# Kernel optimization log

Hardware: AMD Instinct MI355X
Metric: run time of the kernel (lower is better)

## Reference

```python
import jax, jax.numpy as jnp
import numpy as np

E, M, IN, OUT = 8, 8192, 2048, 8192


def setup_inputs() -> dict:
    key = jax.random.key(0)
    k1, k2, k3 = jax.random.split(key, 3)
    inputs = jax.random.normal(k1, (M, IN), dtype=jnp.float32)
    # truncated_normal(-3,3) scaled by init_scale/sqrt(In), matching MoELinear.init
    weight = jax.random.truncated_normal(k2, -3.0, 3.0, (E, IN, OUT), dtype=jnp.float32) * (1.0 / np.sqrt(IN))
    bias = jax.random.normal(k3, (OUT,), dtype=jnp.float32) * 0.02
    # tokens are pre-sorted by expert; balanced routing: M/E tokens per expert
    group_sizes = jnp.full((E,), M // E, dtype=jnp.int32)
    return {"inputs": inputs, "weight": weight, "group_sizes": group_sizes, "bias": bias}


def _ragged_matmul(inputs, weight, group_sizes):
    """Grouped GEMM: out[m] = inputs[m] @ weight[expert_of(m)].

    Tokens are contiguous per expert; group_sizes[e] gives the count for
    expert e. Same math as jax.lax.ragged_dot / megablox gmm.
    """
    n_experts = weight.shape[0]
    m = inputs.shape[0]
    # static-length repeat -> per-token expert id, jit-safe
    expert_ids = jnp.repeat(jnp.arange(n_experts, dtype=group_sizes.dtype),
                            group_sizes, total_repeat_length=m)  # [M]

    def body(acc, ew):
        e, w = ew  # w: [In, Out]
        mask = (expert_ids == e).astype(inputs.dtype)  # [M]
        return acc + (inputs * mask[:, None]) @ w, None

    acc0 = jnp.zeros((m, weight.shape[2]), dtype=inputs.dtype)
    out, _ = jax.lax.scan(body, acc0, (jnp.arange(n_experts, dtype=group_sizes.dtype), weight))
    return out


def reference(inputs, weight, group_sizes, bias):
    # MoELinear.__call__ (ragged_dot path): grouped matmul + bias
    return _ragged_matmul(inputs, weight, group_sizes) + bias
```

## Files before the change

### kernel.cpp

```cpp
#include <hip/hip_runtime.h>
#include <hip/hip_bf16.h>
#include <stdint.h>

#define E_ 8
#define M_ 8192
#define K_ 2048
#define N_ 8192

#define BM 256
#define BN 256
#define BK 64
#define NT (K_ / BK)
#define LDS_BYTES 131072

typedef __attribute__((ext_vector_type(8))) short bf16x8;
typedef __attribute__((ext_vector_type(4))) float f32x4;
typedef __attribute__((ext_vector_type(8))) unsigned short us8;

__device__ __forceinline__ unsigned short f2bf(float f) {
  union { float f; uint32_t u; } v; v.f = f;
  uint32_t u = v.u;
  uint32_t r = (u + 0x7FFFu + ((u >> 16) & 1u)) >> 16;
  return (unsigned short)r;
}

__device__ __forceinline__ unsigned short f2bf_hw(float f) {
  union { __hip_bfloat16 h; unsigned short u; } v;
  v.h = __float2bfloat16(f);
  return v.u;
}

__device__ __forceinline__ void gload_lds16(const void* g, void* l) {
  __builtin_amdgcn_global_load_lds(
      (const __attribute__((address_space(1))) unsigned int*)g,
      (__attribute__((address_space(3))) unsigned int*)l,
      16, 0, 0);
}

__global__ __launch_bounds__(256) void conv_a(const float* __restrict__ A,
                                              unsigned short* __restrict__ Ab,
                                              int n8) {
  int stride = gridDim.x * blockDim.x;
  for (int idx = blockIdx.x * blockDim.x + threadIdx.x; idx < n8; idx += stride) {
    const float4* p = reinterpret_cast<const float4*>(A) + (size_t)idx * 2;
    float4 x0 = p[0], x1 = p[1];
    us8 o;
    o[0] = f2bf(x0.x); o[1] = f2bf(x0.y); o[2] = f2bf(x0.z); o[3] = f2bf(x0.w);
    o[4] = f2bf(x1.x); o[5] = f2bf(x1.y); o[6] = f2bf(x1.z); o[7] = f2bf(x1.w);
    *reinterpret_cast<us8*>(Ab + (size_t)idx * 8) = o;
  }
}

__global__ __launch_bounds__(512, 2) void moe_gemm_fused(
    const unsigned short* __restrict__ Ab,
    const float* __restrict__ W,
    const int* __restrict__ gs,
    const float* __restrict__ bias,
    float* __restrict__ C) {
  extern __shared__ char smem[];

  int tile_n = blockIdx.x;
  int tile_m = blockIdx.y;

  int expert = -1, row_start = 0, rows = 0;
  {
    int acc = 0, off = 0;
    for (int e = 0; e < E_; ++e) {
      int g = gs[e];
      int t = (g + BM - 1) / BM;
      if (expert < 0 && tile_m < acc + t) {
        int lt = tile_m - acc;
        expert = e;
        row_start = off + lt * BM;
        rows = min(BM, g - lt * BM);
      }
      acc += t;
      off += g;
    }
    if (expert < 0) return;
  }

  const float* WfE = W + (size_t)expert * K_ * N_;

  int tid = threadIdx.x;
  int lane = tid & 63;
  int wave = tid >> 6;
  int wr = wave >> 2;
  int wc = wave & 3;
  int bh = wc >> 1;
  int ln15 = lane & 15;
  int n0 = tile_n * BN;

  int slot0 = (((lane >> 4) ^ ((ln15 >> 1) & 7)) << 4);
  int aBase = wr * 16384 + ln15 * 128;
  int bBase = 32768 + bh * 16384 + (wc & 1) * 8192 + ln15 * 128;

  int soff = tid * 16;
  int crow = tid >> 3;
  int lslot = (tid & 7) ^ ((crow >> 1) & 7);
  int scolA = lslot * 8;
  const unsigned short* aS[4];
  #pragma unroll
  for (int c = 0; c < 4; ++c) {
    int r = c * 64 + crow;
    int gr = r < rows ? r : 0;
    aS[c] = Ab + (size_t)(row_start + gr) * K_ + scolA;
  }
#define STG_A(DB, c, kt) \
  gload_lds16(aS[c] + (kt) * 64, smem + (DB) + (c) * 8192 + soff)

  int nB = (tid & 127) * 2;
  int kb0 = tid >> 7;
  const float* wB = WfE + (size_t)(n0 + nB);
  int sB0 = (kb0 ^ ((nB >> 1) & 7)) << 4;
  int sB1 = ((kb0 + 4) ^ ((nB >> 1) & 7)) << 4;
  int bw00 = 32768 + nB * 128 + sB0;
  int bw01 = 32768 + (nB + 1) * 128 + sB0;
  int bw10 = 32768 + nB * 128 + sB1;
  int bw11 = 32768 + (nB + 1) * 128 + sB1;

  float2 fB0[8], fB1[8];

#define LOAD_B(arr, KB, KT)                                                   \
  _Pragma("unroll") for (int j = 0; j < 8; ++j)                               \
    arr[j] = *(const float2*)(wB + (size_t)((KT) * 64 + (KB) * 8 + j) * N_);

#define CVT_WRITE(arr, WE, WO, DBN)                                           \
  do {                                                                        \
    us8 oe, oo;                                                               \
    _Pragma("unroll") for (int p = 0; p < 8; ++p) {                           \
      oe[p] = f2bf_hw(arr[p].x);                                              \
      oo[p] = f2bf_hw(arr[p].y);                                              \
    }                                                                         \
    *(us8*)(smem + (DBN) + (WE)) = oe;                                        \
    *(us8*)(smem + (DBN) + (WO)) = oo;                                        \
  } while (0)

  f32x4 acc4[8][4];
  #pragma unroll
  for (int i = 0; i < 8; ++i)
    #pragma unroll
    for (int j = 0; j < 4; ++j)
      acc4[i][j] = f32x4{0.f, 0.f, 0.f, 0.f};

#define DS_A(frag, DB, MH, KS)                                                \
  _Pragma("unroll") for (int mi = 0; mi < 4; ++mi)                            \
    frag[mi] = *(const bf16x8*)(smem + (DB) + aBase + (MH) * 8192 +           \
                                mi * 2048 + (slot0 ^ ((KS) << 6)));
#define DS_B(frag, DB, KS)                                                    \
  _Pragma("unroll") for (int nj = 0; nj < 4; ++nj)                            \
    frag[nj] = *(const bf16x8*)(smem + (DB) + bBase + nj * 2048 +             \
                                (slot0 ^ ((KS) << 6)));
#define MFMA16(MB, af, bf)                                                    \
  __builtin_amdgcn_s_setprio(1);                                              \
  _Pragma("unroll") for (int mi = 0; mi < 4; ++mi)                            \
    _Pragma("unroll") for (int nj = 0; nj < 4; ++nj)                          \
      acc4[(MB) + mi][nj] = __builtin_amdgcn_mfma_f32_16x16x32_bf16(          \
          af[mi], bf[nj], acc4[(MB) + mi][nj], 0, 0, 0);                      \
  __builtin_amdgcn_s_setprio(0);

#define TILE4(DB, DBN, KTN)                                                   \
  do {                                                                        \
    bf16x8 af[4], bf[4];                                                      \
                                                                      \
    DS_A(af, DB, 0, 0); DS_B(bf, DB, 0);                                      \
    LOAD_B(fB0, kb0, KTN);                                                    \
    __builtin_amdgcn_sched_barrier(0);                                        \
    __builtin_amdgcn_s_barrier();                                             \
    asm volatile("s_waitcnt lgkmcnt(0)" ::: "memory");                        \
    __builtin_amdgcn_sched_barrier(0);                                        \
    MFMA16(0, af, bf);                                                        \
    __builtin_amdgcn_s_barrier();                                             \
                                              \
    DS_A(af, DB, 1, 0);                                                       \
    LOAD_B(fB1, kb0 + 4, KTN);                                                \
    STG_A(DBN, 0, KTN); STG_A(DBN, 1, KTN);                                   \
    STG_A(DBN, 2, KTN); STG_A(DBN, 3, KTN);                                   \
    __builtin_amdgcn_sched_barrier(0);                                        \
    __builtin_amdgcn_s_barrier();                                             \
    asm volatile("s_waitcnt lgkmcnt(0)" ::: "memory");                        \
    __builtin_amdgcn_sched_barrier(0);                                        \
    MFMA16(4, af, bf);                                                        \
    __builtin_amdgcn_s_barrier();                                             \
                                                                      \
    DS_A(af, DB, 0, 1); DS_B(bf, DB, 1);                                      \
    CVT_WRITE(fB0, bw00, bw01, DBN);                                          \
    __builtin_amdgcn_s_barrier();                                             \
    asm volatile("s_waitcnt lgkmcnt(0)" ::: "memory");                        \
    __builtin_amdgcn_sched_barrier(0);                                        \
    MFMA16(0, af, bf);                                                        \
    __builtin_amdgcn_s_barrier();                                             \
                                                                      \
    DS_A(af, DB, 1, 1);                                                       \
    CVT_WRITE(fB1, bw10, bw11, DBN);                                          \
    __builtin_amdgcn_s_barrier();                                             \
    asm volatile("s_waitcnt lgkmcnt(0)" ::: "memory");                        \
    __builtin_amdgcn_sched_barrier(0);                                        \
    MFMA16(4, af, bf);                                                        \
    asm volatile("s_waitcnt vmcnt(0)" ::: "memory");  \
    __builtin_amdgcn_s_barrier();                                             \
  } while (0)

  LOAD_B(fB0, kb0, 0);
  LOAD_B(fB1, kb0 + 4, 0);
  STG_A(0, 0, 0); STG_A(0, 1, 0); STG_A(0, 2, 0); STG_A(0, 3, 0);
  CVT_WRITE(fB0, bw00, bw01, 0);
  CVT_WRITE(fB1, bw10, bw11, 0);
  asm volatile("s_waitcnt vmcnt(0)" ::: "memory");
  asm volatile("s_waitcnt lgkmcnt(0)" ::: "memory");
  __builtin_amdgcn_s_barrier();

  for (int t2 = 0; t2 < NT; t2 += 2) {
    int k2 = (t2 + 2 >= NT) ? 0 : t2 + 2;
    TILE4(0, 65536, t2 + 1);
    TILE4(65536, 0, k2);
  }
#undef TILE4
#undef DS_A
#undef DS_B
#undef MFMA16
#undef STG_A
#undef LOAD_B
#undef CVT_WRITE

  float bv[4];
  #pragma unroll
  for (int nj = 0; nj < 4; ++nj) bv[nj] = bias[n0 + wc * 64 + nj * 16 + ln15];
  #pragma unroll
  for (int mi = 0; mi < 8; ++mi) {
    int r0 = wr * 128 + mi * 16 + (lane >> 4) * 4;
    #pragma unroll
    for (int r = 0; r < 4; ++r) {
      int lr = r0 + r;
      if (lr < rows) {
        float* Cp = C + (size_t)(row_start + lr) * N_ + n0 + wc * 64 + ln15;
        #pragma unroll
        for (int nj = 0; nj < 4; ++nj) Cp[nj * 16] = acc4[mi][nj][r] + bv[nj];
      }
    }
  }
}

__global__ __launch_bounds__(256) void moe_naive(const float* __restrict__ A,
                                                 const float* __restrict__ W,
                                                 const int* __restrict__ gs,
                                                 const float* __restrict__ bias,
                                                 float* __restrict__ C) {
  int col = blockIdx.x * 16 + (threadIdx.x & 15);
  int row = blockIdx.y * 16 + (threadIdx.x >> 4);
  int acc = 0, e = E_ - 1;
  for (int i = 0; i < E_; ++i) {
    int g = gs[i];
    if (row >= acc && row < acc + g) { e = i; break; }
    acc += g;
  }
  const float* a = A + (size_t)row * K_;
  const float* w = W + (size_t)e * K_ * N_ + col;
  float s = 0.f;
  for (int k = 0; k < K_; ++k) s += a[k] * w[(size_t)k * N_];
  C[(size_t)row * N_ + col] = s + bias[col];
}

extern "C" void kernel_launch(void* const* d_in, const int* in_sizes, int n_in,
                              void* d_out, int out_size, void* d_ws, size_t ws_size,
                              hipStream_t stream) {
  const float* A = (const float*)d_in[0];
  const float* W = (const float*)d_in[1];
  const int* gs = (const int*)d_in[2];
  const float* bias = (const float*)d_in[3];
  float* C = (float*)d_out;

  const size_t needA = (size_t)M_ * K_ * 2;

  (void)hipFuncSetAttribute((const void*)moe_gemm_fused,
                            hipFuncAttributeMaxDynamicSharedMemorySize, LDS_BYTES);

  if (ws_size >= needA) {
    unsigned short* Abf = (unsigned short*)d_ws;
    conv_a<<<2048, 256, 0, stream>>>(A, Abf, (M_ * K_) / 8);
    dim3 gg(N_ / BN, M_ / BM + E_);
    moe_gemm_fused<<<gg, 512, LDS_BYTES, stream>>>(Abf, W, gs, bias, C);
  } else {
    dim3 gn(N_ / 16, M_ / 16);
    moe_naive<<<gn, 256, 0, stream>>>(A, W, gs, bias, C);
  }
}
```

Baseline: 441.0 us.

## Prefetch B weights two k-tiles ahead with double register buffers

```diff
diff --git a/kernel.cpp b/kernel.cpp
--- a/kernel.cpp
+++ b/kernel.cpp
@@ -119,7 +119,7 @@
   int bw10 = 32768 + nB * 128 + sB1;
   int bw11 = 32768 + (nB + 1) * 128 + sB1;
 
-  float2 fB0[8], fB1[8];
+  float2 fSA0[8], fSA1[8], fSB0[8], fSB1[8];
 
 #define LOAD_B(arr, KB, KT)                                                   \
   _Pragma("unroll") for (int j = 0; j < 8; ++j)                               \
@@ -159,61 +159,67 @@
           af[mi], bf[nj], acc4[(MB) + mi][nj], 0, 0, 0);                      \
   __builtin_amdgcn_s_setprio(0);
 
-#define TILE4(DB, DBN, KTN)                                                   \
+#define TILE4(DB, DBN, W0, W1, L0, L1, KTA, KTB)                              \
   do {                                                                        \
     bf16x8 af[4], bf[4];                                                      \
-                                                                      \
+                                                             \
     DS_A(af, DB, 0, 0); DS_B(bf, DB, 0);                                      \
-    LOAD_B(fB0, kb0, KTN);                                                    \
+    STG_A(DBN, 0, KTA); STG_A(DBN, 1, KTA);                                   \
+    STG_A(DBN, 2, KTA); STG_A(DBN, 3, KTA);                                   \
+    __builtin_amdgcn_sched_barrier(0);   \
+    LOAD_B(L0, kb0, KTB);                                                     \
     __builtin_amdgcn_sched_barrier(0);                                        \
     __builtin_amdgcn_s_barrier();                                             \
     asm volatile("s_waitcnt lgkmcnt(0)" ::: "memory");                        \
     __builtin_amdgcn_sched_barrier(0);                                        \
     MFMA16(0, af, bf);                                                        \
     __builtin_amdgcn_s_barrier();                                             \
-                                              \
+                                     \
     DS_A(af, DB, 1, 0);                                                       \
-    LOAD_B(fB1, kb0 + 4, KTN);                                                \
-    STG_A(DBN, 0, KTN); STG_A(DBN, 1, KTN);                                   \
-    STG_A(DBN, 2, KTN); STG_A(DBN, 3, KTN);                                   \
+    LOAD_B(L1, kb0 + 4, KTB);                                                 \
     __builtin_amdgcn_sched_barrier(0);                                        \
     __builtin_amdgcn_s_barrier();                                             \
     asm volatile("s_waitcnt lgkmcnt(0)" ::: "memory");                        \
     __builtin_amdgcn_sched_barrier(0);                                        \
     MFMA16(4, af, bf);                                                        \
     __builtin_amdgcn_s_barrier();                                             \
-                                                                      \
+                                           \
     DS_A(af, DB, 0, 1); DS_B(bf, DB, 1);                                      \
-    CVT_WRITE(fB0, bw00, bw01, DBN);                                          \
+    CVT_WRITE(W0, bw00, bw01, DBN);                                           \
     __builtin_amdgcn_s_barrier();                                             \
     asm volatile("s_waitcnt lgkmcnt(0)" ::: "memory");                        \
     __builtin_amdgcn_sched_barrier(0);                                        \
     MFMA16(0, af, bf);                                                        \
     __builtin_amdgcn_s_barrier();                                             \
-                                                                      \
+                                           \
     DS_A(af, DB, 1, 1);                                                       \
-    CVT_WRITE(fB1, bw10, bw11, DBN);                                          \
+    CVT_WRITE(W1, bw10, bw11, DBN);                                           \
     __builtin_amdgcn_s_barrier();                                             \
     asm volatile("s_waitcnt lgkmcnt(0)" ::: "memory");                        \
     __builtin_amdgcn_sched_barrier(0);                                        \
     MFMA16(4, af, bf);                                                        \
-    asm volatile("s_waitcnt vmcnt(0)" ::: "memory");  \
+    asm volatile("s_waitcnt vmcnt(16)" ::: "memory");  \
     __builtin_amdgcn_s_barrier();                                             \
   } while (0)
 
-  LOAD_B(fB0, kb0, 0);
-  LOAD_B(fB1, kb0 + 4, 0);
   STG_A(0, 0, 0); STG_A(0, 1, 0); STG_A(0, 2, 0); STG_A(0, 3, 0);
-  CVT_WRITE(fB0, bw00, bw01, 0);
-  CVT_WRITE(fB1, bw10, bw11, 0);
-  asm volatile("s_waitcnt vmcnt(0)" ::: "memory");
+  __builtin_amdgcn_sched_barrier(0);
+  LOAD_B(fSB0, kb0, 0); LOAD_B(fSB1, kb0 + 4, 0);
+  __builtin_amdgcn_sched_barrier(0);
+  CVT_WRITE(fSB0, bw00, bw01, 0);
+  CVT_WRITE(fSB1, bw10, bw11, 0);
+  LOAD_B(fSA0, kb0, 1); LOAD_B(fSA1, kb0 + 4, 1);
+  __builtin_amdgcn_sched_barrier(0);
   asm volatile("s_waitcnt lgkmcnt(0)" ::: "memory");
   __builtin_amdgcn_s_barrier();
 
   for (int t2 = 0; t2 < NT; t2 += 2) {
-    int k2 = (t2 + 2 >= NT) ? 0 : t2 + 2;
-    TILE4(0, 65536, t2 + 1);
-    TILE4(65536, 0, k2);
+    int ka0 = t2 + 1;
+    int kb0t = (t2 + 2 >= NT) ? 0 : t2 + 2;
+    int ka1 = kb0t;
+    int kb1t = (t2 + 3 >= NT) ? 0 : t2 + 3;
+    TILE4(0, 65536, fSA0, fSA1, fSB0, fSB1, ka0, kb0t);
+    TILE4(65536, 0, fSB0, fSB1, fSA0, fSA1, ka1, kb1t);
   }
 #undef TILE4
 #undef DS_A
@@ -222,6 +228,8 @@
 #undef STG_A
 #undef LOAD_B
 #undef CVT_WRITE
+
+  asm volatile("s_waitcnt vmcnt(0)" ::: "memory");
 
   float bv[4];
   #pragma unroll
```

Result: slower. 499.2 us (+13.2%).
